# Kernel optimization log

Measured on AMD Instinct MI355X. Metric: run time of the kernel, lower is better.

## Reference

```python
import jax, jax.numpy as jnp
import numpy as np

N = 50000      # nodes
E = 500000     # edges
CHAN = 64      # channels
R0 = 2.0       # radial cutoff scale


def radial_encode_8(d, r0):
    # d: (E,) edge distances -> (E, 8) Gaussian radial basis on [0, r0]
    mu = jnp.linspace(0.0, r0, 8).astype(d.dtype)
    sigma = r0 / 8.0
    return jnp.exp(-(((d[:, None] - mu) / sigma) ** 2))


def vector_sigmoid(v):
    # v: (..., 3, chan); sigmoid-shaped vector activation (norm over spatial axis)
    vv = jnp.sum(v * v, axis=-2, keepdims=True)
    return v / jnp.sqrt(1.0 + vv)


def setup_inputs() -> dict:
    key = jax.random.key(0)
    ks = jax.random.split(key, 12)
    rn = lambda i, shape, scale=1.0: jax.random.normal(ks[i], shape, jnp.float32) * scale
    src = jax.random.randint(ks[0], (E,), 0, N)
    dst = jax.random.randint(ks[1], (E,), 0, N)
    r_ij = rn(2, (E, 3))
    z_0 = rn(3, (N, CHAN))
    z_1 = rn(4, (N, 3, CHAN))
    emb = rn(5, (N, CHAN))
    k = CHAN ** -0.5
    return dict(
        src=src, dst=dst, r_ij=r_ij, z_0=z_0, z_1=z_1, emb=emb,
        W_enc=rn(6, (8, CHAN), 8 ** -0.5), b_enc=jnp.zeros((CHAN,), jnp.float32),
        W_src=rn(7, (CHAN, CHAN), k), b_src=jnp.zeros((CHAN,), jnp.float32),
        W_dst=rn(8, (CHAN, CHAN), k), b_dst=jnp.zeros((CHAN,), jnp.float32),
        W_gate=rn(9, (CHAN, 4 * CHAN), k), b_gate=jnp.zeros((4 * CHAN,), jnp.float32),
        W_s=rn(10, (CHAN, CHAN), k), W_v=rn(11, (CHAN, CHAN), k),
    )


def reference(src, dst, r_ij, z_0, z_1, emb,
              W_enc, b_enc, W_src, b_src, W_dst, b_dst,
              W_gate, b_gate, W_s, W_v):
    # edges_read: gather node embeddings to edges, fuse src/dst linears
    emb_ij = (emb[src] @ W_src + b_src) + (emb[dst] @ W_dst + b_dst)        # (E, C)
    d = jnp.sqrt(jnp.sum(r_ij * r_ij, axis=-1))                              # (E,)
    dist_emb = radial_encode_8(d, R0) @ W_enc + b_enc + emb_ij               # (E, C)
    # vector sigmoid on scaled displacement
    r_hat = vector_sigmoid((r_ij * (7.0 / R0))[..., None])[..., 0]           # (E, 3)
    # edges_read_dst: gather dst-node scalar/vector features
    z0_j = z_0[dst]                                                          # (E, C)
    z1_j = z_1[dst]                                                          # (E, 3, C)
    # MessageContract (rank-1 equivariant tensor contraction, gated by dist_emb)
    g = (dist_emb @ W_gate + b_gate).reshape(E, 4, CHAN)                     # (E, 4, C)
    s_msg = g[:, 0] * z0_j + g[:, 1] * jnp.einsum('ei,eic->ec', r_hat, z1_j)  # scalar msg
    psi0 = s_msg @ W_s                                                        # (E, C)
    v_msg = g[:, 2][:, None, :] * z1_j \
          + g[:, 3][:, None, :] * (r_hat[:, :, None] * z0_j[:, None, :])     # (E, 3, C)
    psi1 = jnp.einsum('eic,cd->eid', v_msg, W_v)                              # (E, 3, C)
    # edges_reduce_src: scatter-add messages back to source nodes
    out0 = jax.ops.segment_sum(psi0, src, num_segments=N)                     # (N, C)
    out1 = jax.ops.segment_sum(psi1.reshape(E, 3 * CHAN), src,
                               num_segments=N).reshape(N, 3, CHAN)            # (N, 3, C)
    return out0, out1
```

## Files before the change

### kernel.cpp

```cpp
#include <hip/hip_runtime.h>

typedef unsigned int u32;

#define WS_WSG   0
#define WS_WEG   32768
#define WS_BALL  34816
#define WS_GS    35328

__global__ void zero_k(float* p, int n) {
    int i = blockIdx.x * blockDim.x + threadIdx.x;
    int st = gridDim.x * blockDim.x;
    for (; i < n; i += st) p[i] = 0.0f;
}

__global__ void compose_k(const float* __restrict__ Wsrc, const float* __restrict__ Wdst,
                          const float* __restrict__ Wenc, const float* __restrict__ benc,
                          const float* __restrict__ bsrc, const float* __restrict__ bdst,
                          const float* __restrict__ Wgate, const float* __restrict__ bgate,
                          float* __restrict__ ws) {
    const int j = threadIdx.x;
    const int r = blockIdx.x;
    if (r < 64) {
        float a = 0.f, b = 0.f;
        for (int c = 0; c < 64; ++c) {
            const float wg = Wgate[c * 256 + j];
            a += Wsrc[r * 64 + c] * wg;
            b += Wdst[r * 64 + c] * wg;
        }
        ws[WS_WSG + r * 512 + j] = a;
        ws[WS_WSG + r * 512 + 256 + j] = b;
    } else if (r < 72) {
        const int m = r - 64;
        float a = 0.f;
        for (int c = 0; c < 64; ++c) a += Wenc[m * 64 + c] * Wgate[c * 256 + j];
        ws[WS_WEG + m * 256 + j] = a;
    } else {
        float a = bgate[j];
        for (int c = 0; c < 64; ++c)
            a += (benc[c] + bsrc[c] + bdst[c]) * Wgate[c * 256 + j];
        ws[WS_BALL + j] = a;
    }
}

__global__ __launch_bounds__(512, 1) void nodepre3_k(
    const float* __restrict__ emb, const float* __restrict__ Wc,
    float* __restrict__ G, int N) {
    __shared__ __align__(16) float sW[32768];
    __shared__ __align__(16) float sEm[1024];
    for (int i = threadIdx.x * 4; i < 32768; i += 2048)
        *(float4*)&sW[i] = *(const float4*)&Wc[i];

    const int c4 = (threadIdx.x & 127) << 2;
    const int g = threadIdx.x >> 7;
    const int lim = N * 64;
    const int ntiles = (N + 15) >> 4;

    for (int tile = blockIdx.x; tile < ntiles; tile += gridDim.x) {
        const int n0 = tile << 4;
        const int base = n0 * 64;
        __syncthreads();
        for (int i = threadIdx.x * 4; i < 1024; i += 2048) {
            const int gi = base + i;
            *(float4*)&sEm[i] = (gi < lim) ? *(const float4*)&emb[gi]
                                           : make_float4(0.f, 0.f, 0.f, 0.f);
        }
        for (int i = 2048 + threadIdx.x * 4; i < 1024; i += 2048) { }
        __syncthreads();

        float4 a0 = {0,0,0,0}, a1 = {0,0,0,0}, a2 = {0,0,0,0}, a3 = {0,0,0,0};
        const float* e0p = &sEm[(g * 4 + 0) * 64];
        const float* e1p = &sEm[(g * 4 + 1) * 64];
        const float* e2p = &sEm[(g * 4 + 2) * 64];
        const float* e3p = &sEm[(g * 4 + 3) * 64];
        #pragma unroll 8
        for (int k = 0; k < 64; ++k) {
            const float4 w = *(const float4*)&sW[k * 512 + c4];
            const float e0 = e0p[k], e1 = e1p[k], e2 = e2p[k], e3 = e3p[k];
            a0.x += e0 * w.x; a0.y += e0 * w.y; a0.z += e0 * w.z; a0.w += e0 * w.w;
            a1.x += e1 * w.x; a1.y += e1 * w.y; a1.z += e1 * w.z; a1.w += e1 * w.w;
            a2.x += e2 * w.x; a2.y += e2 * w.y; a2.z += e2 * w.z; a2.w += e2 * w.w;
            a3.x += e3 * w.x; a3.y += e3 * w.y; a3.z += e3 * w.z; a3.w += e3 * w.w;
        }
        const int nb = n0 + g * 4;
        if (nb + 0 < N) *(float4*)&G[(size_t)(nb + 0) * 512 + c4] = a0;
        if (nb + 1 < N) *(float4*)&G[(size_t)(nb + 1) * 512 + c4] = a1;
        if (nb + 2 < N) *(float4*)&G[(size_t)(nb + 2) * 512 + c4] = a2;
        if (nb + 3 < N) *(float4*)&G[(size_t)(nb + 3) * 512 + c4] = a3;
    }
}

__global__ __launch_bounds__(256, 8) void edge_fast_k(
    const int* __restrict__ src, const int* __restrict__ dst,
    const float* __restrict__ r_ij, const float* __restrict__ z0g,
    const float* __restrict__ z1g, const float* __restrict__ G,
    const float* __restrict__ WeG, const float* __restrict__ ball,
    float* __restrict__ out, int N, int E) {
    __shared__ float sWe[2048];
    __shared__ float sBall[256];
    __shared__ int sFl[2];

    if (threadIdx.x == 0) {
        const u32* ps = (const u32*)src;
        const u32* pd = (const u32*)dst;
        int s64 = 1, d64 = 1;
        for (int i = 1; i < 128; i += 2) {
            if (ps[i] != 0u) s64 = 0;
            if (pd[i] != 0u) d64 = 0;
        }
        sFl[0] = s64;
        sFl[1] = d64;
    }
    for (int i = threadIdx.x; i < 2048; i += 256) sWe[i] = WeG[i];
    sBall[threadIdx.x] = ball[threadIdx.x];
    __syncthreads();

    const int wid = threadIdx.x >> 6, lane = threadIdx.x & 63;
    const int i64s = sFl[0], i64d = sFl[1];

    for (int e = blockIdx.x * 4 + wid; e < E; e += gridDim.x * 4) {
        const int s = i64s ? src[2 * e] : src[e];
        const int t = i64d ? dst[2 * e] : dst[e];
        if (s < 0 || s >= N || t < 0 || t >= N) continue;

        const float* gs = G + (size_t)s * 512 + lane;
        const float* gd = G + (size_t)t * 512 + 256 + lane;
        const float a0 = gs[0], a1 = gs[64], a2 = gs[128], a3 = gs[192];
        const float b0 = gd[0], b1 = gd[64], b2 = gd[128], b3 = gd[192];
        const float z0v = z0g[t * 64 + lane];
        const float za = z1g[t * 192 + lane];
        const float zb = z1g[t * 192 + 64 + lane];
        const float zc = z1g[t * 192 + 128 + lane];
        const float r0 = r_ij[e * 3 + 0];
        const float r1 = r_ij[e * 3 + 1];
        const float r2 = r_ij[e * 3 + 2];

        float g0 = a0 + b0 + sBall[lane];
        float g1 = a1 + b1 + sBall[64 + lane];
        float g2 = a2 + b2 + sBall[128 + lane];
        float g3 = a3 + b3 + sBall[192 + lane];

        const float d = sqrtf(r0 * r0 + r1 * r1 + r2 * r2);
        #pragma unroll
        for (int m = 0; m < 8; ++m) {
            const float mu = 0.28571428571f * (float)m;
            const float tt = (d - mu) * 4.0f;
            const float rm = __expf(-tt * tt);
            const float* wq = &sWe[(m << 8) + lane];
            g0 += rm * wq[0];
            g1 += rm * wq[64];
            g2 += rm * wq[128];
            g3 += rm * wq[192];
        }

        const float v0 = r0 * 3.5f, v1 = r1 * 3.5f, v2 = r2 * 3.5f;
        const float inv = rsqrtf(1.0f + v0 * v0 + v1 * v1 + v2 * v2);
        const float h0 = v0 * inv, h1 = v1 * inv, h2 = v2 * inv;
        const float uu = h0 * za + h1 * zb + h2 * zc;

        const float smsg = g0 * z0v + g1 * uu;
        const float vm0 = g2 * za + g3 * h0 * z0v;
        const float vm1 = g2 * zb + g3 * h1 * z0v;
        const float vm2 = g2 * zc + g3 * h2 * z0v;

        atomicAdd(&out[s * 64 + lane], smsg);
        const int bo = N * 64 + s * 192 + lane;
        atomicAdd(&out[bo], vm0);
        atomicAdd(&out[bo + 64], vm1);
        atomicAdd(&out[bo + 128], vm2);
    }
}

__global__ __launch_bounds__(256, 3) void nodepost3_k(
    float* __restrict__ out, const float* __restrict__ Ws,
    const float* __restrict__ Wv, int N) {
    __shared__ __align__(16) float sW[8192];
    __shared__ float sR[64 * 65];
    for (int i = threadIdx.x * 4; i < 8192; i += 1024) {
        *(float4*)&sW[i] = (i < 4096) ? *(const float4*)&Ws[i]
                                      : *(const float4*)&Wv[i - 4096];
    }
    const int c4 = (threadIdx.x & 15) << 2;
    const int rq = threadIdx.x >> 4;
    const int totalRows = 4 * N;
    const int lim = totalRows * 64;
    const int ntiles = (totalRows + 63) >> 6;

    for (int tile = blockIdx.x; tile < ntiles; tile += gridDim.x) {
        const int r0 = tile << 6;
        __syncthreads();
        for (int i = threadIdx.x; i < 4096; i += 256) {
            const int gi = r0 * 64 + i;
            sR[(i >> 6) * 65 + (i & 63)] = (gi < lim) ? out[gi] : 0.f;
        }
        __syncthreads();

        const int rb = rq << 2;
        const int gr = r0 + rb;
        const int o0 = (gr + 0 < N) ? 0 : 4096;
        const int o3 = (gr + 3 < N) ? 0 : 4096;
        float4 a0 = {0,0,0,0}, a1 = {0,0,0,0}, a2 = {0,0,0,0}, a3 = {0,0,0,0};
        const float* rp0 = &sR[(rb + 0) * 65];
        const float* rp1 = &sR[(rb + 1) * 65];
        const float* rp2 = &sR[(rb + 2) * 65];
        const float* rp3 = &sR[(rb + 3) * 65];
        if (o0 == o3) {
            const float* wb = &sW[o0 + c4];
            #pragma unroll 8
            for (int k = 0; k < 64; ++k) {
                const float4 w = *(const float4*)&wb[k * 64];
                const float e0 = rp0[k], e1 = rp1[k], e2 = rp2[k], e3 = rp3[k];
                a0.x += e0 * w.x; a0.y += e0 * w.y; a0.z += e0 * w.z; a0.w += e0 * w.w;
                a1.x += e1 * w.x; a1.y += e1 * w.y; a1.z += e1 * w.z; a1.w += e1 * w.w;
                a2.x += e2 * w.x; a2.y += e2 * w.y; a2.z += e2 * w.z; a2.w += e2 * w.w;
                a3.x += e3 * w.x; a3.y += e3 * w.y; a3.z += e3 * w.z; a3.w += e3 * w.w;
            }
        } else {
            const int o1 = (gr + 1 < N) ? 0 : 4096;
            const int o2 = (gr + 2 < N) ? 0 : 4096;
            #pragma unroll 4
            for (int k = 0; k < 64; ++k) {
                const float4 w0 = *(const float4*)&sW[o0 + k * 64 + c4];
                const float4 w1 = *(const float4*)&sW[o1 + k * 64 + c4];
                const float4 w2 = *(const float4*)&sW[o2 + k * 64 + c4];
                const float4 w3 = *(const float4*)&sW[o3 + k * 64 + c4];
                const float e0 = rp0[k], e1 = rp1[k], e2 = rp2[k], e3 = rp3[k];
                a0.x += e0 * w0.x; a0.y += e0 * w0.y; a0.z += e0 * w0.z; a0.w += e0 * w0.w;
                a1.x += e1 * w1.x; a1.y += e1 * w1.y; a1.z += e1 * w1.z; a1.w += e1 * w1.w;
                a2.x += e2 * w2.x; a2.y += e2 * w2.y; a2.z += e2 * w2.z; a2.w += e2 * w2.w;
                a3.x += e3 * w3.x; a3.y += e3 * w3.y; a3.z += e3 * w3.z; a3.w += e3 * w3.w;
            }
        }
        if (gr + 0 < totalRows) *(float4*)&out[(size_t)(gr + 0) * 64 + c4] = a0;
        if (gr + 1 < totalRows) *(float4*)&out[(size_t)(gr + 1) * 64 + c4] = a1;
        if (gr + 2 < totalRows) *(float4*)&out[(size_t)(gr + 2) * 64 + c4] = a2;
        if (gr + 3 < totalRows) *(float4*)&out[(size_t)(gr + 3) * 64 + c4] = a3;
    }
}

__global__ __launch_bounds__(512, 1) void edge_k(
    const int* __restrict__ src, const int* __restrict__ dst,
    const float* __restrict__ r_ij, const float* __restrict__ z0g,
    const float* __restrict__ z1g, const float* __restrict__ emb,
    const float* __restrict__ Wenc, const float* __restrict__ benc,
    const float* __restrict__ Wsrc, const float* __restrict__ bsrc,
    const float* __restrict__ Wdst, const float* __restrict__ bdst,
    const float* __restrict__ Wgate, const float* __restrict__ bgate,
    const float* __restrict__ Ws, const float* __restrict__ Wv,
    float* __restrict__ out, int N, int E)
{
    __shared__ float sWsrc[4096];
    __shared__ float sWdst[4096];
    __shared__ float sWg[16384];
    __shared__ float sWs[4096];
    __shared__ float sWv[4096];
    __shared__ float sWe[512];
    __shared__ float sB[64];
    __shared__ float sBg[256];
    __shared__ int sFl[2];

    if (threadIdx.x == 0) {
        const u32* ps = (const u32*)src;
        const u32* pd = (const u32*)dst;
        int s64 = 1, d64 = 1;
        for (int i = 1; i < 128; i += 2) {
            if (ps[i] != 0u) s64 = 0;
            if (pd[i] != 0u) d64 = 0;
        }
        sFl[0] = s64;
        sFl[1] = d64;
    }
    for (int i = threadIdx.x; i < 4096; i += 512) {
        sWsrc[i] = Wsrc[i];
        sWdst[i] = Wdst[i];
        sWs[i] = Ws[i];
        sWv[i] = Wv[i];
    }
    for (int i = threadIdx.x; i < 16384; i += 512) sWg[i] = Wgate[i];
    for (int i = threadIdx.x; i < 512; i += 512) sWe[i] = Wenc[i];
    if (threadIdx.x < 64)
        sB[threadIdx.x] = benc[threadIdx.x] + bsrc[threadIdx.x] + bdst[threadIdx.x];
    if (threadIdx.x < 256) sBg[threadIdx.x] = bgate[threadIdx.x];
    __syncthreads();

    const int wid = threadIdx.x >> 6, lane = threadIdx.x & 63;
    const int i64s = sFl[0], i64d = sFl[1];

    for (int e = blockIdx.x * 8 + wid; e < E; e += gridDim.x * 8) {
        const int s = i64s ? src[2 * e] : src[e];
        const int t = i64d ? dst[2 * e] : dst[e];
        if (s < 0 || s >= N || t < 0 || t >= N) continue;

        const float es = emb[s * 64 + lane];
        const float et = emb[t * 64 + lane];
        float de = sB[lane];
        #pragma unroll 8
        for (int k = 0; k < 64; ++k) {
            de += __shfl(es, k, 64) * sWsrc[(k << 6) + lane];
            de += __shfl(et, k, 64) * sWdst[(k << 6) + lane];
        }
        const float r0 = r_ij[e * 3 + 0];
        const float r1 = r_ij[e * 3 + 1];
        const float r2 = r_ij[e * 3 + 2];
        const float d = sqrtf(r0 * r0 + r1 * r1 + r2 * r2);
        #pragma unroll
        for (int m = 0; m < 8; ++m) {
            const float mu = (2.0f / 7.0f) * (float)m;
            const float tt = (d - mu) * 4.0f;
            de += __expf(-tt * tt) * sWe[m * 64 + lane];
        }

        const float v0 = r0 * 3.5f, v1 = r1 * 3.5f, v2 = r2 * 3.5f;
        const float inv = rsqrtf(1.0f + v0 * v0 + v1 * v1 + v2 * v2);
        const float h0 = v0 * inv, h1 = v1 * inv, h2 = v2 * inv;

        const float z0v = z0g[t * 64 + lane];
        const float za = z1g[t * 192 + lane];
        const float zb = z1g[t * 192 + 64 + lane];
        const float zc = z1g[t * 192 + 128 + lane];
        const float uu = h0 * za + h1 * zb + h2 * zc;

        float g0 = sBg[lane], g1 = sBg[64 + lane], g2 = sBg[128 + lane], g3 = sBg[192 + lane];
        #pragma unroll 8
        for (int k = 0; k < 64; ++k) {
            const float dk = __shfl(de, k, 64);
            const float* w = &sWg[(k << 8) + lane];
            g0 += dk * w[0];
            g1 += dk * w[64];
            g2 += dk * w[128];
            g3 += dk * w[192];
        }

        const float smsg = g0 * z0v + g1 * uu;
        const float vm0 = g2 * za + g3 * h0 * z0v;
        const float vm1 = g2 * zb + g3 * h1 * z0v;
        const float vm2 = g2 * zc + g3 * h2 * z0v;

        float p0 = 0.f, q0 = 0.f, q1 = 0.f, q2 = 0.f;
        #pragma unroll 8
        for (int k = 0; k < 64; ++k) {
            const float sk = __shfl(smsg, k, 64);
            const float a = __shfl(vm0, k, 64);
            const float b = __shfl(vm1, k, 64);
            const float c = __shfl(vm2, k, 64);
            p0 += sk * sWs[(k << 6) + lane];
            const float wv = sWv[(k << 6) + lane];
            q0 += a * wv;
            q1 += b * wv;
            q2 += c * wv;
        }

        atomicAdd(&out[s * 64 + lane], p0);
        const int b1 = N * 64 + s * 192 + lane;
        atomicAdd(&out[b1], q0);
        atomicAdd(&out[b1 + 64], q1);
        atomicAdd(&out[b1 + 128], q2);
    }
}

extern "C" void kernel_launch(void* const* d_in, const int* in_sizes, int n_in,
                              void* d_out, int out_size, void* d_ws, size_t ws_size,
                              hipStream_t stream) {
    const int* src = (const int*)d_in[0];
    const int* dst = (const int*)d_in[1];
    const float* r_ij = (const float*)d_in[2];
    const float* z0g  = (const float*)d_in[3];
    const float* z1g  = (const float*)d_in[4];
    const float* emb  = (const float*)d_in[5];
    const float* Wenc = (const float*)d_in[6];
    const float* benc = (const float*)d_in[7];
    const float* Wsrc = (const float*)d_in[8];
    const float* bsrc = (const float*)d_in[9];
    const float* Wdst = (const float*)d_in[10];
    const float* bdst = (const float*)d_in[11];
    const float* Wgate = (const float*)d_in[12];
    const float* bgate = (const float*)d_in[13];
    const float* Ws = (const float*)d_in[14];
    const float* Wv = (const float*)d_in[15];

    const int N = out_size / 256;
    int E = in_sizes[0];
    if (in_sizes[2] / 3 < E) E = in_sizes[2] / 3;

    zero_k<<<2048, 256, 0, stream>>>((float*)d_out, out_size);

    float* ws = (float*)d_ws;
    const size_t need = ((size_t)WS_GS + (size_t)N * 512u) * sizeof(float);

    if (ws != nullptr && ws_size >= need) {
        compose_k<<<73, 256, 0, stream>>>(Wsrc, Wdst, Wenc, benc, bsrc, bdst,
                                          Wgate, bgate, ws);
        float* G = ws + WS_GS;
        nodepre3_k<<<256, 512, 0, stream>>>(emb, ws + WS_WSG, G, N);
        edge_fast_k<<<2048, 256, 0, stream>>>(src, dst, r_ij, z0g, z1g, G,
                                              ws + WS_WEG, ws + WS_BALL,
                                              (float*)d_out, N, E);
        nodepost3_k<<<2048, 256, 0, stream>>>((float*)d_out, Ws, Wv, N);
    } else {
        edge_k<<<2048, 512, 0, stream>>>(src, dst, r_ij, z0g, z1g, emb, Wenc, benc,
                                         Wsrc, bsrc, Wdst, bdst, Wgate, bgate, Ws, Wv,
                                         (float*)d_out, N, E);
    }
}
```

Before: 677.6 us.

## Sort edges by source into CSR and reduce per node without atomics

Adds a counting-sort pipeline (count, single-block scan, fill) that builds a CSR table of edges grouped by source node, with packed r_ij and dst per entry. A new edge kernel assigns one wavefront per source node, accumulates messages in registers and writes each output row once. This removes the zeroing of the output and the float atomic scatter-adds. In exchange it adds several kernels, a serial single-block scan, and atomic counters during the build. Edge order within a row depends on the atomics, so float summation order can vary between runs.

```diff
diff --git a/kernel.cpp b/kernel.cpp
--- a/kernel.cpp
+++ b/kernel.cpp
@@ -64,7 +64,6 @@
             *(float4*)&sEm[i] = (gi < lim) ? *(const float4*)&emb[gi]
                                            : make_float4(0.f, 0.f, 0.f, 0.f);
         }
-        for (int i = 2048 + threadIdx.x * 4; i < 1024; i += 2048) { }
         __syncthreads();
 
         float4 a0 = {0,0,0,0}, a1 = {0,0,0,0}, a2 = {0,0,0,0}, a3 = {0,0,0,0};
@@ -86,6 +85,163 @@
         if (nb + 1 < N) *(float4*)&G[(size_t)(nb + 1) * 512 + c4] = a1;
         if (nb + 2 < N) *(float4*)&G[(size_t)(nb + 2) * 512 + c4] = a2;
         if (nb + 3 < N) *(float4*)&G[(size_t)(nb + 3) * 512 + c4] = a3;
+    }
+}
+
+__global__ void count_k(const int* __restrict__ src, const int* __restrict__ dst,
+                        int* __restrict__ cnt, int N, int E) {
+    __shared__ int sFl[2];
+    if (threadIdx.x == 0) {
+        const u32* ps = (const u32*)src;
+        const u32* pd = (const u32*)dst;
+        int s64 = 1, d64 = 1;
+        for (int i = 1; i < 128; i += 2) {
+            if (ps[i] != 0u) s64 = 0;
+            if (pd[i] != 0u) d64 = 0;
+        }
+        sFl[0] = s64;
+        sFl[1] = d64;
+    }
+    __syncthreads();
+    const int i64s = sFl[0], i64d = sFl[1];
+    for (int e = blockIdx.x * blockDim.x + threadIdx.x; e < E;
+         e += gridDim.x * blockDim.x) {
+        const int s = i64s ? src[2 * e] : src[e];
+        const int t = i64d ? dst[2 * e] : dst[e];
+        if (s < 0 || s >= N || t < 0 || t >= N) continue;
+        atomicAdd(&cnt[s], 1);
+    }
+}
+
+__global__ __launch_bounds__(1024) void scan_k(int* __restrict__ cnt, int N) {
+    __shared__ int sp[1024];
+    const int tid = threadIdx.x;
+    const int chunk = (N + 1023) >> 10;
+    const int beg = tid * chunk;
+    int end = beg + chunk; if (end > N) end = N;
+    int sum = 0;
+    for (int i = beg; i < end; ++i) sum += cnt[i];
+    sp[tid] = sum;
+    __syncthreads();
+    for (int off = 1; off < 1024; off <<= 1) {
+        const int v = (tid >= off) ? sp[tid - off] : 0;
+        __syncthreads();
+        sp[tid] += v;
+        __syncthreads();
+    }
+    int cur = (tid == 0) ? 0 : sp[tid - 1];
+    for (int i = beg; i < end; ++i) {
+        const int c = cnt[i];
+        cnt[i] = cur;
+        cur += c;
+    }
+}
+
+__global__ void fill_k(const int* __restrict__ src, const int* __restrict__ dst,
+                       const float* __restrict__ r_ij, int* __restrict__ cursor,
+                       float4* __restrict__ tbl, int N, int E) {
+    __shared__ int sFl[2];
+    if (threadIdx.x == 0) {
+        const u32* ps = (const u32*)src;
+        const u32* pd = (const u32*)dst;
+        int s64 = 1, d64 = 1;
+        for (int i = 1; i < 128; i += 2) {
+            if (ps[i] != 0u) s64 = 0;
+            if (pd[i] != 0u) d64 = 0;
+        }
+        sFl[0] = s64;
+        sFl[1] = d64;
+    }
+    __syncthreads();
+    const int i64s = sFl[0], i64d = sFl[1];
+    for (int e = blockIdx.x * blockDim.x + threadIdx.x; e < E;
+         e += gridDim.x * blockDim.x) {
+        const int s = i64s ? src[2 * e] : src[e];
+        const int t = i64d ? dst[2 * e] : dst[e];
+        if (s < 0 || s >= N || t < 0 || t >= N) continue;
+        const float r0 = r_ij[e * 3 + 0];
+        const float r1 = r_ij[e * 3 + 1];
+        const float r2 = r_ij[e * 3 + 2];
+        const int pos = atomicAdd(&cursor[s], 1);
+        tbl[pos] = make_float4(r0, r1, r2, __int_as_float(t));
+    }
+}
+
+__global__ __launch_bounds__(256, 8) void edge_csr_k(
+    const float* __restrict__ G, const float* __restrict__ z0g,
+    const float* __restrict__ z1g, const int* __restrict__ rowend,
+    const float4* __restrict__ tbl, const float* __restrict__ WeG,
+    const float* __restrict__ ball, float* __restrict__ out, int N) {
+    __shared__ float sWe[2048];
+    __shared__ float sBall[256];
+    for (int i = threadIdx.x; i < 2048; i += 256) sWe[i] = WeG[i];
+    sBall[threadIdx.x] = ball[threadIdx.x];
+    __syncthreads();
+
+    const int wid = threadIdx.x >> 6, lane = threadIdx.x & 63;
+    const int w = blockIdx.x * 4 + wid;
+    const int nw = gridDim.x * 4;
+
+    const float bl0 = sBall[lane], bl1 = sBall[64 + lane];
+    const float bl2 = sBall[128 + lane], bl3 = sBall[192 + lane];
+
+    for (int n = w; n < N; n += nw) {
+        const int beg = (n == 0) ? 0 : rowend[n - 1];
+        const int end = rowend[n];
+
+        const float* gs = G + (size_t)n * 512 + lane;
+        const float gsb0 = gs[0]   + bl0;
+        const float gsb1 = gs[64]  + bl1;
+        const float gsb2 = gs[128] + bl2;
+        const float gsb3 = gs[192] + bl3;
+
+        float accS = 0.f, accV0 = 0.f, accV1 = 0.f, accV2 = 0.f;
+
+        for (int i = beg; i < end; ++i) {
+            const float4 mt = tbl[i];
+            const int t = __float_as_int(mt.w);
+            const float r0 = mt.x, r1 = mt.y, r2 = mt.z;
+
+            const float* gd = G + (size_t)t * 512 + 256 + lane;
+            const float b0 = gd[0], b1 = gd[64], b2 = gd[128], b3 = gd[192];
+            const float z0v = z0g[t * 64 + lane];
+            const float* zp = z1g + t * 192 + lane;
+            const float za = zp[0], zb = zp[64], zc = zp[128];
+
+            float g0 = gsb0 + b0;
+            float g1 = gsb1 + b1;
+            float g2 = gsb2 + b2;
+            float g3 = gsb3 + b3;
+
+            const float d = sqrtf(r0 * r0 + r1 * r1 + r2 * r2);
+            #pragma unroll
+            for (int m = 0; m < 8; ++m) {
+                const float mu = 0.28571428571f * (float)m;
+                const float tt = (d - mu) * 4.0f;
+                const float rm = __expf(-tt * tt);
+                const float* wq = &sWe[(m << 8) + lane];
+                g0 += rm * wq[0];
+                g1 += rm * wq[64];
+                g2 += rm * wq[128];
+                g3 += rm * wq[192];
+            }
+
+            const float v0 = r0 * 3.5f, v1 = r1 * 3.5f, v2 = r2 * 3.5f;
+            const float inv = rsqrtf(1.0f + v0 * v0 + v1 * v1 + v2 * v2);
+            const float h0 = v0 * inv, h1 = v1 * inv, h2 = v2 * inv;
+            const float uu = h0 * za + h1 * zb + h2 * zc;
+
+            accS  += g0 * z0v + g1 * uu;
+            accV0 += g2 * za + g3 * h0 * z0v;
+            accV1 += g2 * zb + g3 * h1 * z0v;
+            accV2 += g2 * zc + g3 * h2 * z0v;
+        }
+
+        out[n * 64 + lane] = accS;
+        const int bo = N * 64 + n * 192 + lane;
+        out[bo] = accV0;
+        out[bo + 64] = accV1;
+        out[bo + 128] = accV2;
     }
 }
 
@@ -381,21 +537,38 @@
     int E = in_sizes[0];
     if (in_sizes[2] / 3 < E) E = in_sizes[2] / 3;
 
-    zero_k<<<2048, 256, 0, stream>>>((float*)d_out, out_size);
-
     float* ws = (float*)d_ws;
-    const size_t need = ((size_t)WS_GS + (size_t)N * 512u) * sizeof(float);
-
-    if (ws != nullptr && ws_size >= need) {
+    const size_t gsz = (size_t)N * 512u;
+    const size_t needG   = ((size_t)WS_GS + gsz) * sizeof(float);
+    const size_t tblOff  = (size_t)WS_GS + gsz;
+    const size_t cntOff  = tblOff + 4u * (size_t)E;
+    const size_t needCSR = (cntOff + (size_t)N + 16u) * sizeof(float);
+
+    if (ws != nullptr && ws_size >= needG) {
         compose_k<<<73, 256, 0, stream>>>(Wsrc, Wdst, Wenc, benc, bsrc, bdst,
                                           Wgate, bgate, ws);
         float* G = ws + WS_GS;
         nodepre3_k<<<256, 512, 0, stream>>>(emb, ws + WS_WSG, G, N);
-        edge_fast_k<<<2048, 256, 0, stream>>>(src, dst, r_ij, z0g, z1g, G,
-                                              ws + WS_WEG, ws + WS_BALL,
-                                              (float*)d_out, N, E);
+
+        if (ws_size >= needCSR) {
+            float4* tbl = (float4*)(ws + tblOff);
+            int* cnt = (int*)(ws + cntOff);
+            zero_k<<<64, 256, 0, stream>>>((float*)cnt, N);
+            count_k<<<1024, 256, 0, stream>>>(src, dst, cnt, N, E);
+            scan_k<<<1, 1024, 0, stream>>>(cnt, N);
+            fill_k<<<1024, 256, 0, stream>>>(src, dst, r_ij, cnt, tbl, N, E);
+            edge_csr_k<<<2048, 256, 0, stream>>>(G, z0g, z1g, cnt, tbl,
+                                                 ws + WS_WEG, ws + WS_BALL,
+                                                 (float*)d_out, N);
+        } else {
+            zero_k<<<2048, 256, 0, stream>>>((float*)d_out, out_size);
+            edge_fast_k<<<2048, 256, 0, stream>>>(src, dst, r_ij, z0g, z1g, G,
+                                                  ws + WS_WEG, ws + WS_BALL,
+                                                  (float*)d_out, N, E);
+        }
         nodepost3_k<<<2048, 256, 0, stream>>>((float*)d_out, Ws, Wv, N);
     } else {
+        zero_k<<<2048, 256, 0, stream>>>((float*)d_out, out_size);
         edge_k<<<2048, 512, 0, stream>>>(src, dst, r_ij, z0g, z1g, emb, Wenc, benc,
                                          Wsrc, bsrc, Wdst, bdst, Wgate, bgate, Ws, Wv,
                                          (float*)d_out, N, E);
```

Result: slower. 891.1 us (+31.5%).

## Store per-node gate projections and dst features as interleaved fp16 for edge gathers

Applied to the files above, without the earlier changes.

Node-level gate projections (G) are now written in fp16 with the four gate channels interleaved per lane, and a new kernel packs z_1 and z_0 for each node into one interleaved fp16 array. The edge kernel then gathers three 8-byte vectors per lane instead of twelve scalar fp32 loads. This is meant to cut the bytes moved by the random per-edge gathers, which dominate the cost. In exchange it adds an extra packing pass and loses precision, which could break the accuracy tolerance.

```diff
diff --git a/kernel.cpp b/kernel.cpp
--- a/kernel.cpp
+++ b/kernel.cpp
@@ -1,6 +1,8 @@
 #include <hip/hip_runtime.h>
 
 typedef unsigned int u32;
+typedef _Float16 h16;
+typedef __attribute__((ext_vector_type(4))) _Float16 h4;
 
 #define WS_WSG   0
 #define WS_WEG   32768
@@ -20,6 +22,7 @@
                           float* __restrict__ ws) {
     const int j = threadIdx.x;
     const int r = blockIdx.x;
+    const int p = ((j & 63) << 2) + (j >> 6);
     if (r < 64) {
         float a = 0.f, b = 0.f;
         for (int c = 0; c < 64; ++c) {
@@ -27,8 +30,8 @@
             a += Wsrc[r * 64 + c] * wg;
             b += Wdst[r * 64 + c] * wg;
         }
-        ws[WS_WSG + r * 512 + j] = a;
-        ws[WS_WSG + r * 512 + 256 + j] = b;
+        ws[WS_WSG + r * 512 + p] = a;
+        ws[WS_WSG + r * 512 + 256 + p] = b;
     } else if (r < 72) {
         const int m = r - 64;
         float a = 0.f;
@@ -44,7 +47,7 @@
 
 __global__ __launch_bounds__(512, 1) void nodepre3_k(
     const float* __restrict__ emb, const float* __restrict__ Wc,
-    float* __restrict__ G, int N) {
+    h16* __restrict__ HG, int N) {
     __shared__ __align__(16) float sW[32768];
     __shared__ __align__(16) float sEm[1024];
     for (int i = threadIdx.x * 4; i < 32768; i += 2048)
@@ -64,7 +67,6 @@
             *(float4*)&sEm[i] = (gi < lim) ? *(const float4*)&emb[gi]
                                            : make_float4(0.f, 0.f, 0.f, 0.f);
         }
-        for (int i = 2048 + threadIdx.x * 4; i < 1024; i += 2048) { }
         __syncthreads();
 
         float4 a0 = {0,0,0,0}, a1 = {0,0,0,0}, a2 = {0,0,0,0}, a3 = {0,0,0,0};
@@ -82,19 +84,34 @@
             a3.x += e3 * w.x; a3.y += e3 * w.y; a3.z += e3 * w.z; a3.w += e3 * w.w;
         }
         const int nb = n0 + g * 4;
-        if (nb + 0 < N) *(float4*)&G[(size_t)(nb + 0) * 512 + c4] = a0;
-        if (nb + 1 < N) *(float4*)&G[(size_t)(nb + 1) * 512 + c4] = a1;
-        if (nb + 2 < N) *(float4*)&G[(size_t)(nb + 2) * 512 + c4] = a2;
-        if (nb + 3 < N) *(float4*)&G[(size_t)(nb + 3) * 512 + c4] = a3;
-    }
-}
-
-__global__ __launch_bounds__(256, 8) void edge_fast_k(
+        const h4 h0 = { (h16)a0.x, (h16)a0.y, (h16)a0.z, (h16)a0.w };
+        const h4 h1 = { (h16)a1.x, (h16)a1.y, (h16)a1.z, (h16)a1.w };
+        const h4 h2 = { (h16)a2.x, (h16)a2.y, (h16)a2.z, (h16)a2.w };
+        const h4 h3 = { (h16)a3.x, (h16)a3.y, (h16)a3.z, (h16)a3.w };
+        if (nb + 0 < N) *(h4*)&HG[(size_t)(nb + 0) * 512 + c4] = h0;
+        if (nb + 1 < N) *(h4*)&HG[(size_t)(nb + 1) * 512 + c4] = h1;
+        if (nb + 2 < N) *(h4*)&HG[(size_t)(nb + 2) * 512 + c4] = h2;
+        if (nb + 3 < N) *(h4*)&HG[(size_t)(nb + 3) * 512 + c4] = h3;
+    }
+}
+
+__global__ void hz_k(const float* __restrict__ z0g, const float* __restrict__ z1g,
+                     h16* __restrict__ HZ, int N) {
+    const int tot = N * 64;
+    for (int idx = blockIdx.x * blockDim.x + threadIdx.x; idx < tot;
+         idx += gridDim.x * blockDim.x) {
+        const int n = idx >> 6, l = idx & 63;
+        const h4 v = { (h16)z1g[n * 192 + l], (h16)z1g[n * 192 + 64 + l],
+                       (h16)z1g[n * 192 + 128 + l], (h16)z0g[n * 64 + l] };
+        *(h4*)&HZ[(size_t)n * 256 + (l << 2)] = v;
+    }
+}
+
+__global__ __launch_bounds__(256, 8) void edge_h16_k(
     const int* __restrict__ src, const int* __restrict__ dst,
-    const float* __restrict__ r_ij, const float* __restrict__ z0g,
-    const float* __restrict__ z1g, const float* __restrict__ G,
-    const float* __restrict__ WeG, const float* __restrict__ ball,
-    float* __restrict__ out, int N, int E) {
+    const float* __restrict__ r_ij, const h16* __restrict__ HG,
+    const h16* __restrict__ HZ, const float* __restrict__ WeG,
+    const float* __restrict__ ball, float* __restrict__ out, int N, int E) {
     __shared__ float sWe[2048];
     __shared__ float sBall[256];
     __shared__ int sFl[2];
@@ -117,27 +134,27 @@
     const int wid = threadIdx.x >> 6, lane = threadIdx.x & 63;
     const int i64s = sFl[0], i64d = sFl[1];
 
+    const float bl0 = sBall[lane], bl1 = sBall[64 + lane];
+    const float bl2 = sBall[128 + lane], bl3 = sBall[192 + lane];
+
     for (int e = blockIdx.x * 4 + wid; e < E; e += gridDim.x * 4) {
         const int s = i64s ? src[2 * e] : src[e];
         const int t = i64d ? dst[2 * e] : dst[e];
         if (s < 0 || s >= N || t < 0 || t >= N) continue;
 
-        const float* gs = G + (size_t)s * 512 + lane;
-        const float* gd = G + (size_t)t * 512 + 256 + lane;
-        const float a0 = gs[0], a1 = gs[64], a2 = gs[128], a3 = gs[192];
-        const float b0 = gd[0], b1 = gd[64], b2 = gd[128], b3 = gd[192];
-        const float z0v = z0g[t * 64 + lane];
-        const float za = z1g[t * 192 + lane];
-        const float zb = z1g[t * 192 + 64 + lane];
-        const float zc = z1g[t * 192 + 128 + lane];
+        const h4 gsv = *(const h4*)&HG[(size_t)s * 512 + (lane << 2)];
+        const h4 gdv = *(const h4*)&HG[(size_t)t * 512 + 256 + (lane << 2)];
+        const h4 zv  = *(const h4*)&HZ[(size_t)t * 256 + (lane << 2)];
         const float r0 = r_ij[e * 3 + 0];
         const float r1 = r_ij[e * 3 + 1];
         const float r2 = r_ij[e * 3 + 2];
 
-        float g0 = a0 + b0 + sBall[lane];
-        float g1 = a1 + b1 + sBall[64 + lane];
-        float g2 = a2 + b2 + sBall[128 + lane];
-        float g3 = a3 + b3 + sBall[192 + lane];
+        float g0 = (float)gsv.x + (float)gdv.x + bl0;
+        float g1 = (float)gsv.y + (float)gdv.y + bl1;
+        float g2 = (float)gsv.z + (float)gdv.z + bl2;
+        float g3 = (float)gsv.w + (float)gdv.w + bl3;
+        const float za = (float)zv.x, zb = (float)zv.y, zc = (float)zv.z;
+        const float z0v = (float)zv.w;
 
         const float d = sqrtf(r0 * r0 + r1 * r1 + r2 * r2);
         #pragma unroll
@@ -384,16 +401,18 @@
     zero_k<<<2048, 256, 0, stream>>>((float*)d_out, out_size);
 
     float* ws = (float*)d_ws;
-    const size_t need = ((size_t)WS_GS + (size_t)N * 512u) * sizeof(float);
+    const size_t need = ((size_t)WS_GS + (size_t)N * 384u + 16u) * sizeof(float);
 
     if (ws != nullptr && ws_size >= need) {
         compose_k<<<73, 256, 0, stream>>>(Wsrc, Wdst, Wenc, benc, bsrc, bdst,
                                           Wgate, bgate, ws);
-        float* G = ws + WS_GS;
-        nodepre3_k<<<256, 512, 0, stream>>>(emb, ws + WS_WSG, G, N);
-        edge_fast_k<<<2048, 256, 0, stream>>>(src, dst, r_ij, z0g, z1g, G,
-                                              ws + WS_WEG, ws + WS_BALL,
-                                              (float*)d_out, N, E);
+        h16* HG = (h16*)(ws + WS_GS);
+        h16* HZ = HG + (size_t)N * 512;
+        nodepre3_k<<<256, 512, 0, stream>>>(emb, ws + WS_WSG, HG, N);
+        hz_k<<<1024, 256, 0, stream>>>(z0g, z1g, HZ, N);
+        edge_h16_k<<<2048, 256, 0, stream>>>(src, dst, r_ij, HG, HZ,
+                                             ws + WS_WEG, ws + WS_BALL,
+                                             (float*)d_out, N, E);
         nodepost3_k<<<2048, 256, 0, stream>>>((float*)d_out, Ws, Wv, N);
     } else {
         edge_k<<<2048, 512, 0, stream>>>(src, dst, r_ij, z0g, z1g, emb, Wenc, benc,
```

Measured after the change: 676.2 us. About the same (-0.2%).
